# Kernel tuning notes

Hardware: AMD Instinct MI355X
Metric: run time of the kernel (lower is better)

Reference implementation:

```python
import jax, jax.numpy as jnp
import numpy as np

N, S, F, E, H, O, L, FE = 8, 1024, 64, 512, 8, 64, 6, 4
HD = E // H
FF = FE * E


def setup_inputs() -> dict:
    key = jax.random.key(0)
    ks = iter(jax.random.split(key, 40))
    def rn(shape, s=0.02):
        return jax.random.normal(next(ks), shape, jnp.float32) * s
    return {
        'x': jax.random.normal(next(ks), (N, F, S), jnp.float32),
        'W_first': rn((F, E)), 'b_first': jnp.zeros((E,), jnp.float32),
        'pos_emb': rn((S, E)),
        'Wq': rn((L, HD, HD)), 'bq': jnp.zeros((L, HD), jnp.float32),
        'Wk': rn((L, HD, HD)), 'bk': jnp.zeros((L, HD), jnp.float32),
        'Wv': rn((L, HD, HD)), 'bv': jnp.zeros((L, HD), jnp.float32),
        'Wo': rn((L, E, E)), 'bo': jnp.zeros((L, E), jnp.float32),
        'g1': jnp.ones((L, E), jnp.float32), 'be1': jnp.zeros((L, E), jnp.float32),
        'Wf1': rn((L, E, FF)), 'bf1': jnp.zeros((L, FF), jnp.float32),
        'Wf2': rn((L, FF, E)), 'bf2': jnp.zeros((L, E), jnp.float32),
        'g2': jnp.ones((L, E), jnp.float32), 'be2': jnp.zeros((L, E), jnp.float32),
        'Wfin': rn((E, O)), 'bfin': jnp.zeros((O,), jnp.float32),
    }


def layernorm(x, g, b, eps=1e-5):
    m = jnp.mean(x, axis=-1, keepdims=True)
    v = jnp.mean(jnp.square(x - m), axis=-1, keepdims=True)
    return (x - m) * jax.lax.rsqrt(v + eps) * g + b


def reference(x, W_first, b_first, pos_emb, Wq, bq, Wk, bk, Wv, bv, Wo, bo,
              g1, be1, Wf1, bf1, Wf2, bf2, g2, be2, Wfin, bfin):
    # x: (N, F, S) -> (N, S, F)
    h = jax.nn.relu(jnp.einsum('nfs,fe->nse', x, W_first) + b_first) + pos_emb[None]
    scale = E ** 0.5  # note: module scales by sqrt(embed_size), not sqrt(head_dim)
    for i in range(L):
        t = h.reshape(N, S, H, HD)
        q = jnp.einsum('nshd,de->nshe', t, Wq[i]) + bq[i]
        k = jnp.einsum('nshd,de->nshe', t, Wk[i]) + bk[i]
        v = jnp.einsum('nshd,de->nshe', t, Wv[i]) + bv[i]
        energy = jnp.einsum('nqhd,nkhd->nhqk', q, k)  # (N,H,S,S)
        att = jax.nn.softmax(energy / scale, axis=-1)
        o = jnp.einsum('nhqk,nkhd->nqhd', att, v).reshape(N, S, E)
        o = jnp.einsum('nse,ef->nsf', o, Wo[i]) + bo[i]
        hx = layernorm(o + h, g1[i], be1[i])
        ff = jax.nn.relu(jnp.einsum('nse,ef->nsf', hx, Wf1[i]) + bf1[i])
        ff = jnp.einsum('nsf,fe->nse', ff, Wf2[i]) + bf2[i]
        h = layernorm(ff + hx, g2[i], be2[i])
    # Conv1d kernel_size=1 == pointwise linear over channels; output (N, O, S)
    return jnp.einsum('nse,eo->nos', h, Wfin) + bfin[None, :, None]
```

## Files before the change

kernel.cpp:

```cpp
#include <hip/hip_runtime.h>
#include <hip/hip_bf16.h>
#include <math.h>

#define N_ 8
#define S_ 1024
#define F_ 64
#define E_ 512
#define H_ 8
#define O_ 64
#define L_ 6
#define HD_ 64
#define FF_ 2048
#define SCALE_ 0.044194173824159216f
#define LOG2E_ 1.4426950408889634f
#define QSCALE_ (SCALE_ * LOG2E_)

typedef unsigned short u16;
typedef __attribute__((ext_vector_type(4))) unsigned short u16x4;
typedef __attribute__((ext_vector_type(8))) unsigned short u16x8;
typedef __attribute__((ext_vector_type(8))) short short8;
typedef __attribute__((ext_vector_type(4))) float floatx4;

__device__ __forceinline__ u16 f2b(float f) {
    union { float f; unsigned u; } v; v.f = f;
    unsigned u = v.u;
    unsigned r = (u + 0x7FFFu + ((u >> 16) & 1u)) >> 16;
    return (u16)r;
}
__device__ __forceinline__ u16 f2b_fast(float f) {
    union { float f; unsigned u; } v; v.f = f;
    return (u16)((v.u + 0x8000u) >> 16);
}
__device__ __forceinline__ float b2f(u16 h) {
    union { unsigned u; float f; } v; v.u = ((unsigned)h) << 16;
    return v.f;
}

__device__ __forceinline__ void gload16(const u16* g, u16* l) {
    __builtin_amdgcn_global_load_lds(
        (const __attribute__((address_space(1))) void*)g,
        (__attribute__((address_space(3))) void*)l, 16, 0, 0);
}

__global__ __launch_bounds__(256) void first_mfma(
    const float* __restrict__ x, const u16* __restrict__ wt,
    const float* __restrict__ bf, const float* __restrict__ pe,
    u16* __restrict__ resb)
{
    __shared__ u16 a_s[128][72];
    int t = threadIdx.x;
    int w = t >> 6, lane = t & 63, quad = lane >> 4, c16 = lane & 15;
    int rowhalf = w >> 1, colhalf = w & 1;
    int col0 = blockIdx.x * 128;
    int row0 = blockIdx.y * 128;
    int n = row0 >> 10, s0 = row0 & 1023;

    const float* xb = x + (size_t)n * F_ * S_ + s0;
    #pragma unroll
    for (int i = 0; i < 8; i++) {
        int pos = (t + i * 256) * 4;
        int f = pos >> 7, sl = pos & 127;
        float4 v = *(const float4*)&xb[(size_t)f * S_ + sl];
        a_s[sl + 0][f] = f2b_fast(v.x);
        a_s[sl + 1][f] = f2b_fast(v.y);
        a_s[sl + 2][f] = f2b_fast(v.z);
        a_s[sl + 3][f] = f2b_fast(v.w);
    }
    __syncthreads();

    floatx4 acc[4][4];
    #pragma unroll
    for (int mt = 0; mt < 4; mt++)
        #pragma unroll
        for (int nt = 0; nt < 4; nt++) acc[mt][nt] = (floatx4){0.f, 0.f, 0.f, 0.f};

    #pragma unroll
    for (int ks = 0; ks < 2; ks++) {
        short8 af[4], bfr[4];
        #pragma unroll
        for (int mt = 0; mt < 4; mt++)
            af[mt] = *(const short8*)&a_s[rowhalf * 64 + mt * 16 + c16][ks * 32 + quad * 8];
        #pragma unroll
        for (int nt = 0; nt < 4; nt++)
            bfr[nt] = *(const short8*)&wt[(size_t)(col0 + colhalf * 64 + nt * 16 + c16) * F_
                                          + ks * 32 + quad * 8];
        #pragma unroll
        for (int mt = 0; mt < 4; mt++)
            #pragma unroll
            for (int nt = 0; nt < 4; nt++)
                acc[mt][nt] = __builtin_amdgcn_mfma_f32_16x16x32_bf16(
                    af[mt], bfr[nt], acc[mt][nt], 0, 0, 0);
    }

    #pragma unroll
    for (int nt = 0; nt < 4; nt++) {
        int col = col0 + colhalf * 64 + nt * 16 + c16;
        float bv = bf[col];
        #pragma unroll
        for (int mt = 0; mt < 4; mt++) {
            #pragma unroll
            for (int r = 0; r < 4; r++) {
                size_t row = (size_t)row0 + rowhalf * 64 + mt * 16 + quad * 4 + r;
                int s = (int)(row & 1023);
                float v = fmaxf(acc[mt][nt][r] + bv, 0.f) + pe[(size_t)s * E_ + col];
                resb[row * E_ + col] = f2b_fast(v);
            }
        }
    }
}

__global__ __launch_bounds__(256) void wprep(
    const float* __restrict__ W_first, const float* __restrict__ Wo,
    const float* __restrict__ Wf1, const float* __restrict__ Wf2,
    const float* __restrict__ Wfin,
    const float* __restrict__ Wq, const float* __restrict__ Wk,
    const float* __restrict__ Wv,
    u16* __restrict__ w1t, u16* __restrict__ wot, u16* __restrict__ wf1t,
    u16* __restrict__ wf2t, u16* __restrict__ wft,
    u16* __restrict__ wqt, u16* __restrict__ wkt, u16* __restrict__ wvt)
{
    int b = blockIdx.x;
    int t = threadIdx.x;
    __shared__ float tile[32][33];
    const float* W; u16* Wt; int K, Nc, bx, by;
    if (b < 32) {
        W = W_first; Wt = w1t; K = F_; Nc = E_; bx = b & 15; by = b >> 4;
    } else if (b < 32 + 1536) {
        int i = b - 32; int z = i >> 8; int r = i & 255;
        W = Wo + (size_t)z * E_ * E_; Wt = wot + (size_t)z * E_ * E_;
        K = E_; Nc = E_; bx = r & 15; by = r >> 4;
    } else if (b < 32 + 1536 + 6144) {
        int i = b - (32 + 1536); int z = i >> 10; int r = i & 1023;
        W = Wf1 + (size_t)z * E_ * FF_; Wt = wf1t + (size_t)z * E_ * FF_;
        K = E_; Nc = FF_; bx = r & 63; by = r >> 6;
    } else if (b < 32 + 1536 + 12288) {
        int i = b - (32 + 1536 + 6144); int z = i >> 10; int r = i & 1023;
        W = Wf2 + (size_t)z * FF_ * E_; Wt = wf2t + (size_t)z * FF_ * E_;
        K = FF_; Nc = E_; bx = r & 15; by = r >> 4;
    } else if (b < 32 + 1536 + 12288 + 32) {
        int r = b - (32 + 1536 + 12288);
        W = Wfin; Wt = wft; K = E_; Nc = O_; bx = r & 1; by = r >> 1;
    } else {
        int l = b - (32 + 1536 + 12288 + 32);
        size_t off = (size_t)l * HD_ * HD_;
        #pragma unroll
        for (int i = 0; i < 16; i++) {
            int idx = t + i * 256;
            int e = idx >> 6, d = idx & 63;
            wqt[off + idx] = f2b(Wq[off + d * HD_ + e]);
            wkt[off + idx] = f2b(Wk[off + d * HD_ + e]);
            wvt[off + idx] = f2b(Wv[off + d * HD_ + e]);
        }
        return;
    }
    #pragma unroll
    for (int i = 0; i < 4; i++) {
        int q = t + i * 256; int r = q >> 5, c = q & 31;
        tile[r][c] = W[(size_t)(by * 32 + r) * Nc + bx * 32 + c];
    }
    __syncthreads();
    #pragma unroll
    for (int i = 0; i < 4; i++) {
        int q = t + i * 256; int r = q >> 5, c = q & 31;
        Wt[(size_t)(bx * 32 + r) * K + by * 32 + c] = f2b(tile[c][r]);
    }
}

__global__ __launch_bounds__(256) void qkv_mfma(
    const u16* __restrict__ hb,
    const u16* __restrict__ wqt, const u16* __restrict__ wkt,
    const u16* __restrict__ wvt,
    const float* __restrict__ bq, const float* __restrict__ bk,
    const float* __restrict__ bvp,
    u16* __restrict__ qo, u16* __restrict__ ko, u16* __restrict__ vt)
{
    __shared__ u16 a_s[128 * 64];
    int t = threadIdx.x;
    int w = t >> 6, lane = t & 63, quad = lane >> 4, c16 = lane & 15;
    size_t row0 = (size_t)blockIdx.x * 128;

    #pragma unroll
    for (int i = 0; i < 4; i++) {
        int q = t + i * 256; int r = q >> 3, c = q & 7;
        *(u16x8*)&a_s[r * 64 + ((c ^ (r & 7)) * 8)] =
            *(const u16x8*)&hb[(row0 + r) * HD_ + c * 8];
    }
    __syncthreads();

    short8 af[2][2];
    #pragma unroll
    for (int mt = 0; mt < 2; mt++)
        #pragma unroll
        for (int ks = 0; ks < 2; ks++) {
            int r = w * 32 + mt * 16 + c16;
            af[mt][ks] = *(const short8*)&a_s[r * 64 + (((ks * 4 + quad) ^ (r & 7)) * 8)];
        }

    const u16* wts[2] = {wqt, wkt};
    const float* bs[2] = {bq, bk};
    u16* outs[2] = {qo, ko};
    #pragma unroll
    for (int m = 0; m < 2; m++) {
        short8 bfr[4][2];
        #pragma unroll
        for (int nt = 0; nt < 4; nt++)
            #pragma unroll
            for (int ks = 0; ks < 2; ks++)
                bfr[nt][ks] = *(const short8*)&wts[m][(nt * 16 + c16) * HD_ + ks * 32 + quad * 8];
        floatx4 acc[2][4];
        #pragma unroll
        for (int mt = 0; mt < 2; mt++)
            #pragma unroll
            for (int nt = 0; nt < 4; nt++) acc[mt][nt] = (floatx4){0.f, 0.f, 0.f, 0.f};
        #pragma unroll
        for (int ks = 0; ks < 2; ks++)
            #pragma unroll
            for (int mt = 0; mt < 2; mt++)
                #pragma unroll
                for (int nt = 0; nt < 4; nt++)
                    acc[mt][nt] = __builtin_amdgcn_mfma_f32_16x16x32_bf16(
                        af[mt][ks], bfr[nt][ks], acc[mt][nt], 0, 0, 0);
        float osc = (m == 0) ? QSCALE_ : 1.0f;
        #pragma unroll
        for (int nt = 0; nt < 4; nt++) {
            float bv_ = bs[m][nt * 16 + c16];
            #pragma unroll
            for (int mt = 0; mt < 2; mt++)
                #pragma unroll
                for (int r = 0; r < 4; r++)
                    outs[m][(row0 + w * 32 + mt * 16 + quad * 4 + r) * HD_ + nt * 16 + c16] =
                        f2b_fast((acc[mt][nt][r] + bv_) * osc);
        }
    }

    {
        short8 bfr[4][2];
        #pragma unroll
        for (int nt = 0; nt < 4; nt++)
            #pragma unroll
            for (int ks = 0; ks < 2; ks++)
                bfr[nt][ks] = *(const short8*)&wvt[(nt * 16 + c16) * HD_ + ks * 32 + quad * 8];
        floatx4 acc[2][4];
        #pragma unroll
        for (int mt = 0; mt < 2; mt++)
            #pragma unroll
            for (int nt = 0; nt < 4; nt++) acc[mt][nt] = (floatx4){0.f, 0.f, 0.f, 0.f};
        #pragma unroll
        for (int ks = 0; ks < 2; ks++)
            #pragma unroll
            for (int mt = 0; mt < 2; mt++)
                #pragma unroll
                for (int nt = 0; nt < 4; nt++)
                    acc[mt][nt] = __builtin_amdgcn_mfma_f32_16x16x32_bf16(
                        af[mt][ks], bfr[nt][ks], acc[mt][nt], 0, 0, 0);

        __syncthreads();
        u16* vt_s = a_s;
        #pragma unroll
        for (int nt = 0; nt < 4; nt++) {
            float bv_ = bvp[nt * 16 + c16];
            #pragma unroll
            for (int mt = 0; mt < 2; mt++)
                #pragma unroll
                for (int r = 0; r < 4; r++) {
                    int fr = w * 32 + mt * 16 + quad * 4 + r;
                    int h = fr & 7, sl = fr >> 3;
                    vt_s[((h * 64 + nt * 16 + c16) * 16) + sl] =
                        f2b_fast(acc[mt][nt][r] + bv_);
                }
        }
        __syncthreads();
        int sflat0 = (int)(row0 >> 3);
        int n = sflat0 >> 10, sbase = sflat0 & 1023;
        #pragma unroll
        for (int i = 0; i < 4; i++) {
            int u = t + i * 256;
            int h = u >> 7, rest = u & 127, d = rest >> 1, half = rest & 1;
            *(u16x8*)&vt[((size_t)((n * 8 + h) * 64 + d)) * (size_t)S_ + sbase + half * 8] =
                *(u16x8*)&vt_s[(h * 64 + d) * 16 + half * 8];
        }
    }
}

__global__ __launch_bounds__(256, 4) void attn_mfma(
    const u16* __restrict__ Q, const u16* __restrict__ K,
    const u16* __restrict__ Vt, u16* __restrict__ O)
{
    int bid0 = blockIdx.x;
    int bid = (bid0 & 7) * 128 + (bid0 >> 3);
    int qt = bid & 15, hh = (bid >> 4) & 7, n = bid >> 7;
    int t = threadIdx.x;
    int w = t >> 6, lane = t & 63, quad = lane >> 4, c16 = lane & 15;

    __shared__ u16 qp_s[64 * 64];
    __shared__ u16 k_s[2][64 * 64];
    __shared__ u16 vt_s[2][64 * 64];
    u16* p_s = qp_s + w * 16 * 64;

    const size_t qkbase = (size_t)n * S_ * E_ + hh * 64;
    const size_t vtbase = ((size_t)(n * H_ + hh) * 64) * (size_t)S_;

    int ar = t >> 3, act = t & 7;
    int acq = act * 8;
    int scw[2];
    #pragma unroll
    for (int i = 0; i < 2; i++) scw[i] = ((act ^ ((ar + i * 32) & 7)) * 8);

    #pragma unroll
    for (int i = 0; i < 2; i++) {
        int q = t + i * 256; int r = q >> 3, c = q & 7;
        *(u16x8*)&qp_s[r * 64 + ((c ^ (r & 7)) * 8)] =
            *(const u16x8*)&Q[qkbase + (size_t)(qt * 64 + r) * E_ + c * 8];
    }
    u16x8 pk[2], pv[2];
    #pragma unroll
    for (int i = 0; i < 2; i++) {
        pk[i] = *(const u16x8*)&K[qkbase + (size_t)(ar + i * 32) * E_ + acq];
        pv[i] = *(const u16x8*)&Vt[vtbase + (size_t)(ar + i * 32) * S_ + acq];
    }
    __syncthreads();

    short8 qf[2];
    #pragma unroll
    for (int ks = 0; ks < 2; ks++) {
        int r = w * 16 + c16;
        qf[ks] = *(const short8*)&qp_s[r * 64 + (((ks * 4 + quad) ^ (r & 7)) * 8)];
    }

    #pragma unroll
    for (int i = 0; i < 2; i++) {
        int r = ar + i * 32;
        *(u16x8*)&k_s[0][r * 64 + scw[i]] = pk[i];
        *(u16x8*)&vt_s[0][r * 64 + scw[i]] = pv[i];
    }
    __syncthreads();

    const short8 ones = {(short)0x3F80, (short)0x3F80, (short)0x3F80, (short)0x3F80,
                         (short)0x3F80, (short)0x3F80, (short)0x3F80, (short)0x3F80};

    floatx4 oaccT[4];
    floatx4 lacc = (floatx4){0.f, 0.f, 0.f, 0.f};
    #pragma unroll
    for (int mt = 0; mt < 4; mt++) oaccT[mt] = (floatx4){0.f, 0.f, 0.f, 0.f};

    for (int k0 = 0; k0 < S_; k0 += 64) {
        int cur = (k0 >> 6) & 1;
        const u16* ks_ = k_s[cur];
        const u16* vs_ = vt_s[cur];
        bool more = (k0 + 64 < S_);
        if (more) {
            #pragma unroll
            for (int i = 0; i < 2; i++) {
                pk[i] = *(const u16x8*)&K[qkbase + (size_t)(k0 + 64 + ar + i * 32) * E_ + acq];
                pv[i] = *(const u16x8*)&Vt[vtbase + (size_t)(ar + i * 32) * S_ + k0 + 64 + acq];
            }
        }

        floatx4 st[4];
        #pragma unroll
        for (int mt = 0; mt < 4; mt++) st[mt] = (floatx4){0.f, 0.f, 0.f, 0.f};
        __builtin_amdgcn_s_setprio(1);
        #pragma unroll
        for (int ks = 0; ks < 2; ks++) {
            short8 kf[4];
            #pragma unroll
            for (int mt = 0; mt < 4; mt++) {
                int r = mt * 16 + c16;
                kf[mt] = *(const short8*)&ks_[r * 64 + (((ks * 4 + quad) ^ (r & 7)) * 8)];
            }
            #pragma unroll
            for (int mt = 0; mt < 4; mt++)
                st[mt] = __builtin_amdgcn_mfma_f32_16x16x32_bf16(
                    kf[mt], qf[ks], st[mt], 0, 0, 0);
        }
        __builtin_amdgcn_s_setprio(0);

        #pragma unroll
        for (int mt = 0; mt < 4; mt++) {
            u16x4 h;
            #pragma unroll
            for (int r = 0; r < 4; r++) h[r] = f2b_fast(exp2f(st[mt][r]));
            *(u16x4*)&p_s[c16 * 64 + (((2 * mt + (quad >> 1)) ^ (c16 & 7)) * 8)
                          + (quad & 1) * 4] = h;
        }

        __builtin_amdgcn_s_setprio(1);
        #pragma unroll
        for (int ks = 0; ks < 2; ks++) {
            short8 pf = *(const short8*)&p_s[c16 * 64 + (((ks * 4 + quad) ^ (c16 & 7)) * 8)];
            short8 vf[4];
            #pragma unroll
            for (int mt = 0; mt < 4; mt++) {
                int r = mt * 16 + c16;
                vf[mt] = *(const short8*)&vs_[r * 64 + (((ks * 4 + quad) ^ (r & 7)) * 8)];
            }
            lacc = __builtin_amdgcn_mfma_f32_16x16x32_bf16(ones, pf, lacc, 0, 0, 0);
            #pragma unroll
            for (int mt = 0; mt < 4; mt++)
                oaccT[mt] = __builtin_amdgcn_mfma_f32_16x16x32_bf16(
                    vf[mt], pf, oaccT[mt], 0, 0, 0);
        }
        __builtin_amdgcn_s_setprio(0);

        if (more) {
            u16* kd = k_s[cur ^ 1];
            u16* vd = vt_s[cur ^ 1];
            #pragma unroll
            for (int i = 0; i < 2; i++) {
                int r = ar + i * 32;
                *(u16x8*)&kd[r * 64 + scw[i]] = pk[i];
                *(u16x8*)&vd[r * 64 + scw[i]] = pv[i];
            }
        }
        __syncthreads();
    }

    {
        float rl = 1.f / lacc[0];
        int s = qt * 64 + w * 16 + c16;
        size_t base = (size_t)(n * S_ + s) * E_ + hh * 64;
        #pragma unroll
        for (int mt = 0; mt < 4; mt++) {
            u16x4 h;
            #pragma unroll
            for (int r = 0; r < 4; r++) h[r] = f2b_fast(oaccT[mt][r] * rl);
            *(u16x4*)&O[base + mt * 16 + quad * 4] = h;
        }
    }
}

template <int MT, int NT, bool RELU, bool HASRES, bool OUTF32, bool OUTBF16>
__global__ __launch_bounds__(256, 2) void gemm_mfma(
    const u16* __restrict__ A, const u16* __restrict__ Bt,
    const float* __restrict__ bias, const u16* __restrict__ resid,
    float* __restrict__ outf, u16* __restrict__ outb, int M, int Nc, int K)
{
    constexpr int MFR = MT / 32;
    constexpr int NFR = NT / 32;
    constexpr int AI  = MT / 32;
    constexpr int BI  = NT / 32;
    __shared__ u16 a_s[MT * 64];
    __shared__ u16 b_s[NT * 64];

    int t = threadIdx.x;
    int w = t >> 6, lane = t & 63, quad = lane >> 4, c16 = lane & 15;
    int rw = w >> 1, cw = w & 1;

    int gx = gridDim.x;
    int nwg = gx * (int)gridDim.y;
    int lin = (int)blockIdx.y * gx + (int)blockIdx.x;
    int cpx = nwg >> 3;
    int id2 = (lin & 7) * cpx + (lin >> 3);
    int bx = id2 % gx, by = id2 / gx;

    size_t row0 = (size_t)by * MT;
    size_t col0 = (size_t)bx * NT;

    size_t aoff[AI]; int adst[AI];
    #pragma unroll
    for (int i = 0; i < AI; i++) {
        int p = t + i * 256;
        int r = p >> 3;
        int kc = (p & 7) ^ (r & 7);
        aoff[i] = (row0 + r) * (size_t)K + kc * 8;
        adst[i] = w * 512 + i * 2048;
    }
    size_t boff[BI]; int bdst[BI];
    #pragma unroll
    for (int i = 0; i < BI; i++) {
        int p = t + i * 256;
        int r = p >> 3;
        int kc = (p & 7) ^ (r & 7);
        boff[i] = (col0 + r) * (size_t)K + kc * 8;
        bdst[i] = w * 512 + i * 2048;
    }

    floatx4 acc[MFR][NFR];
    #pragma unroll
    for (int mt = 0; mt < MFR; mt++)
        #pragma unroll
        for (int nt = 0; nt < NFR; nt++) acc[mt][nt] = (floatx4){0.f, 0.f, 0.f, 0.f};

    for (int k0 = 0; k0 < K; k0 += 64) {
        #pragma unroll
        for (int i = 0; i < AI; i++) gload16(A + aoff[i] + k0, a_s + adst[i]);
        #pragma unroll
        for (int i = 0; i < BI; i++) gload16(Bt + boff[i] + k0, b_s + bdst[i]);
        __syncthreads();

        #pragma unroll
        for (int ks = 0; ks < 2; ks++) {
            short8 af[MFR], bfr[NFR];
            #pragma unroll
            for (int mt = 0; mt < MFR; mt++) {
                int r = rw * (MT / 2) + mt * 16 + c16;
                af[mt] = *(const short8*)&a_s[r * 64 + (((ks * 4 + quad) ^ (r & 7)) * 8)];
            }
            #pragma unroll
            for (int nt = 0; nt < NFR; nt++) {
                int r = cw * (NT / 2) + nt * 16 + c16;
                bfr[nt] = *(const short8*)&b_s[r * 64 + (((ks * 4 + quad) ^ (r & 7)) * 8)];
            }
            #pragma unroll
            for (int mt = 0; mt < MFR; mt++)
                #pragma unroll
                for (int nt = 0; nt < NFR; nt++)
                    acc[mt][nt] = __builtin_amdgcn_mfma_f32_16x16x32_bf16(
                        af[mt], bfr[nt], acc[mt][nt], 0, 0, 0);
        }
        __syncthreads();
    }

    #pragma unroll
    for (int nt = 0; nt < NFR; nt++) {
        int col = (int)col0 + cw * (NT / 2) + nt * 16 + c16;
        float bv = bias[col];
        #pragma unroll
        for (int mt = 0; mt < MFR; mt++) {
            size_t rowb = row0 + rw * (MT / 2) + mt * 16 + quad * 4;
            #pragma unroll
            for (int r = 0; r < 4; r++) {
                size_t row = rowb + r;
                float v = acc[mt][nt][r] + bv;
                if constexpr (HASRES) v += b2f(resid[row * Nc + col]);
                if constexpr (RELU) v = fmaxf(v, 0.f);
                if constexpr (OUTF32) outf[row * Nc + col] = v;
                if constexpr (OUTBF16) outb[row * Nc + col] = f2b_fast(v);
            }
        }
    }
}

__global__ __launch_bounds__(256) void layernorm_k(
    const float* __restrict__ in, const float* __restrict__ g,
    const float* __restrict__ bb, u16* __restrict__ outb)
{
    int row = blockIdx.x;
    int t = threadIdx.x;
    const float* x = in + (size_t)row * E_;
    float x0 = x[t], x1 = x[t + 256];
    float s = x0 + x1;
    #pragma unroll
    for (int off = 32; off; off >>= 1) s += __shfl_down(s, off, 64);
    __shared__ float red[4];
    int wid = t >> 6, lane = t & 63;
    if (lane == 0) red[wid] = s;
    __syncthreads();
    float m = (red[0] + red[1] + red[2] + red[3]) * (1.f / E_);
    float d0 = x0 - m, d1 = x1 - m;
    float sq = d0 * d0 + d1 * d1;
    #pragma unroll
    for (int off = 32; off; off >>= 1) sq += __shfl_down(sq, off, 64);
    __syncthreads();
    if (lane == 0) red[wid] = sq;
    __syncthreads();
    float var = (red[0] + red[1] + red[2] + red[3]) * (1.f / E_);
    float rstd = rsqrtf(var + 1e-5f);
    outb[(size_t)row * E_ + t] = f2b_fast(d0 * rstd * g[t] + bb[t]);
    outb[(size_t)row * E_ + t + 256] = f2b_fast(d1 * rstd * g[t + 256] + bb[t + 256]);
}

__global__ __launch_bounds__(256) void final_mfma(
    const u16* __restrict__ hb, const u16* __restrict__ wft,
    const float* __restrict__ bfin, float* __restrict__ outp)
{
    __shared__ u16 a_s[64][72];
    int t = threadIdx.x;
    int w = t >> 6, lane = t & 63, quad = lane >> 4, c16 = lane & 15;
    size_t row0 = (size_t)blockIdx.x * 64;

    floatx4 acc[4];
    #pragma unroll
    for (int nt = 0; nt < 4; nt++) acc[nt] = (floatx4){0.f, 0.f, 0.f, 0.f};

    int ar = t >> 3, acq = (t & 7) * 8;
    u16x8 pa[2];
    #pragma unroll
    for (int i = 0; i < 2; i++)
        pa[i] = *(const u16x8*)&hb[(row0 + ar + i * 32) * E_ + acq];

    for (int k0 = 0; k0 < E_; k0 += 64) {
        #pragma unroll
        for (int i = 0; i < 2; i++)
            *(u16x8*)&a_s[ar + i * 32][acq] = pa[i];
        __syncthreads();
        if (k0 + 64 < E_) {
            #pragma unroll
            for (int i = 0; i < 2; i++)
                pa[i] = *(const u16x8*)&hb[(row0 + ar + i * 32) * E_ + k0 + 64 + acq];
        }
        #pragma unroll
        for (int ks = 0; ks < 2; ks++) {
            short8 af = *(const short8*)&a_s[w * 16 + c16][ks * 32 + quad * 8];
            #pragma unroll
            for (int nt = 0; nt < 4; nt++) {
                short8 bf = *(const short8*)&wft[(nt * 16 + c16) * E_ + k0 + ks * 32 + quad * 8];
                acc[nt] = __builtin_amdgcn_mfma_f32_16x16x32_bf16(af, bf, acc[nt], 0, 0, 0);
            }
        }
        __syncthreads();
    }

    #pragma unroll
    for (int nt = 0; nt < 4; nt++) {
        int o = nt * 16 + c16;
        float bv = bfin[o];
        #pragma unroll
        for (int r = 0; r < 4; r++) {
            size_t row = row0 + w * 16 + quad * 4 + r;
            int n = (int)(row >> 10), s = (int)(row & 1023);
            outp[((size_t)(n * O_ + o)) * S_ + s] = acc[nt][r] + bv;
        }
    }
}

extern "C" void kernel_launch(void* const* d_in, const int* in_sizes, int n_in,
                              void* d_out, int out_size, void* d_ws, size_t ws_size,
                              hipStream_t stream)
{
    const float* x       = (const float*)d_in[0];
    const float* W_first = (const float*)d_in[1];
    const float* b_first = (const float*)d_in[2];
    const float* pos_emb = (const float*)d_in[3];
    const float* Wq      = (const float*)d_in[4];
    const float* bq      = (const float*)d_in[5];
    const float* Wk      = (const float*)d_in[6];
    const float* bk      = (const float*)d_in[7];
    const float* Wv      = (const float*)d_in[8];
    const float* bv      = (const float*)d_in[9];
    const float* Wo      = (const float*)d_in[10];
    const float* bo      = (const float*)d_in[11];
    const float* g1      = (const float*)d_in[12];
    const float* be1     = (const float*)d_in[13];
    const float* Wf1     = (const float*)d_in[14];
    const float* bf1     = (const float*)d_in[15];
    const float* Wf2     = (const float*)d_in[16];
    const float* bf2     = (const float*)d_in[17];
    const float* g2      = (const float*)d_in[18];
    const float* be2     = (const float*)d_in[19];
    const float* Wfin    = (const float*)d_in[20];
    const float* bfin    = (const float*)d_in[21];
    float* out = (float*)d_out;

    const size_t M4 = (size_t)N_ * S_ * E_;
    float* t1   = (float*)d_ws;
    u16*   resb = (u16*)(t1 + M4);
    u16*   qb   = resb + M4;
    u16*   kb   = qb + M4;
    u16*   vt   = kb + M4;
    u16*   ob   = vt + M4;
    u16*   ffb  = qb;
    u16*   wot  = ob + M4;
    u16*   wf1t = wot + (size_t)L_ * E_ * E_;
    u16*   wf2t = wf1t + (size_t)L_ * E_ * FF_;
    u16*   wqt  = wf2t + (size_t)L_ * FF_ * E_;
    u16*   wkt  = wqt + (size_t)L_ * HD_ * HD_;
    u16*   wvt  = wkt + (size_t)L_ * HD_ * HD_;
    u16*   wft  = wvt + (size_t)L_ * HD_ * HD_;
    u16*   w1t  = wft + (size_t)O_ * E_;

    const int rows = N_ * S_;

    wprep<<<32 + 1536 + 12288 + 32 + 6, 256, 0, stream>>>(
        W_first, Wo, Wf1, Wf2, Wfin, Wq, Wk, Wv,
        w1t, wot, wf1t, wf2t, wft, wqt, wkt, wvt);

    first_mfma<<<dim3(E_ / 128, rows / 128), 256, 0, stream>>>(
        x, w1t, b_first, pos_emb, resb);

    for (int i = 0; i < L_; i++) {
        qkv_mfma<<<512, 256, 0, stream>>>(
            resb, wqt + (size_t)i * HD_ * HD_, wkt + (size_t)i * HD_ * HD_,
            wvt + (size_t)i * HD_ * HD_, bq + i * HD_, bk + i * HD_, bv + i * HD_,
            qb, kb, vt);
        attn_mfma<<<1024, 256, 0, stream>>>(qb, kb, vt, ob);
        gemm_mfma<128, 64, false, true, true, false><<<dim3(E_ / 64, rows / 128), 256, 0, stream>>>(
            ob, wot + (size_t)i * E_ * E_, bo + i * E_, resb, t1, nullptr, rows, E_, E_);
        layernorm_k<<<rows, 256, 0, stream>>>(t1, g1 + i * E_, be1 + i * E_, resb);
        gemm_mfma<128, 128, true, false, false, true><<<dim3(FF_ / 128, rows / 128), 256, 0, stream>>>(
            resb, wf1t + (size_t)i * E_ * FF_, bf1 + i * FF_, nullptr, nullptr, ffb,
            rows, FF_, E_);
        gemm_mfma<128, 64, false, true, true, false><<<dim3(E_ / 64, rows / 128), 256, 0, stream>>>(
            ffb, wf2t + (size_t)i * FF_ * E_, bf2 + i * E_, resb, t1, nullptr,
            rows, E_, FF_);
        layernorm_k<<<rows, 256, 0, stream>>>(t1, g2 + i * E_, be2 + i * E_, resb);
    }

    final_mfma<<<rows / 64, 256, 0, stream>>>(resb, wft, bfin, out);
}
```

Before: 1.005 ms.

## Double-buffer GEMM loads, widen attention blocks, vectorize layernorm, simplify QKV loads

The GEMM kernel now double-buffers its A/B shared tiles so the next K-slice loads are issued before the current slice's MFMAs, removing one barrier per iteration. Attention blocks grow to 512 threads covering 128 query rows, so each K/V tile staged in shared memory serves twice as many queries and each thread issues half as many tile loads. The QKV kernel reads its A fragments straight from global memory and no longer stages them in LDS, dropping a barrier. Layernorm uses float2 loads and packed bf16 stores. The costs are doubled GEMM shared memory, which may lower occupancy, and launch_bounds(512,4), which may constrain registers in the attention kernel.

```diff
diff --git a/kernel.cpp b/kernel.cpp
--- a/kernel.cpp
+++ b/kernel.cpp
@@ -174,27 +174,18 @@
     const float* __restrict__ bvp,
     u16* __restrict__ qo, u16* __restrict__ ko, u16* __restrict__ vt)
 {
-    __shared__ u16 a_s[128 * 64];
+    __shared__ u16 vt_s[128 * 64];
     int t = threadIdx.x;
     int w = t >> 6, lane = t & 63, quad = lane >> 4, c16 = lane & 15;
     size_t row0 = (size_t)blockIdx.x * 128;
 
-    #pragma unroll
-    for (int i = 0; i < 4; i++) {
-        int q = t + i * 256; int r = q >> 3, c = q & 7;
-        *(u16x8*)&a_s[r * 64 + ((c ^ (r & 7)) * 8)] =
-            *(const u16x8*)&hb[(row0 + r) * HD_ + c * 8];
-    }
-    __syncthreads();
-
     short8 af[2][2];
     #pragma unroll
     for (int mt = 0; mt < 2; mt++)
         #pragma unroll
-        for (int ks = 0; ks < 2; ks++) {
-            int r = w * 32 + mt * 16 + c16;
-            af[mt][ks] = *(const short8*)&a_s[r * 64 + (((ks * 4 + quad) ^ (r & 7)) * 8)];
-        }
+        for (int ks = 0; ks < 2; ks++)
+            af[mt][ks] = *(const short8*)&hb[(row0 + w * 32 + mt * 16 + c16) * HD_
+                                             + ks * 32 + quad * 8];
 
     const u16* wts[2] = {wqt, wkt};
     const float* bs[2] = {bq, bk};
@@ -254,8 +245,6 @@
                     acc[mt][nt] = __builtin_amdgcn_mfma_f32_16x16x32_bf16(
                         af[mt][ks], bfr[nt][ks], acc[mt][nt], 0, 0, 0);
 
-        __syncthreads();
-        u16* vt_s = a_s;
         #pragma unroll
         for (int nt = 0; nt < 4; nt++) {
             float bv_ = bvp[nt * 16 + c16];
@@ -282,17 +271,17 @@
     }
 }
 
-__global__ __launch_bounds__(256, 4) void attn_mfma(
+__global__ __launch_bounds__(512, 4) void attn_mfma(
     const u16* __restrict__ Q, const u16* __restrict__ K,
     const u16* __restrict__ Vt, u16* __restrict__ O)
 {
     int bid0 = blockIdx.x;
-    int bid = (bid0 & 7) * 128 + (bid0 >> 3);
-    int qt = bid & 15, hh = (bid >> 4) & 7, n = bid >> 7;
+    int bid = (bid0 & 7) * 64 + (bid0 >> 3);
+    int qt = bid & 7, hh = (bid >> 3) & 7, n = bid >> 6;
     int t = threadIdx.x;
     int w = t >> 6, lane = t & 63, quad = lane >> 4, c16 = lane & 15;
 
-    __shared__ u16 qp_s[64 * 64];
+    __shared__ u16 qp_s[128 * 64];
     __shared__ u16 k_s[2][64 * 64];
     __shared__ u16 vt_s[2][64 * 64];
     u16* p_s = qp_s + w * 16 * 64;
@@ -302,22 +291,16 @@
 
     int ar = t >> 3, act = t & 7;
     int acq = act * 8;
-    int scw[2];
-    #pragma unroll
-    for (int i = 0; i < 2; i++) scw[i] = ((act ^ ((ar + i * 32) & 7)) * 8);
+    int scw = (act ^ (ar & 7)) * 8;
 
     #pragma unroll
     for (int i = 0; i < 2; i++) {
-        int q = t + i * 256; int r = q >> 3, c = q & 7;
+        int q = t + i * 512; int r = q >> 3, c = q & 7;
         *(u16x8*)&qp_s[r * 64 + ((c ^ (r & 7)) * 8)] =
-            *(const u16x8*)&Q[qkbase + (size_t)(qt * 64 + r) * E_ + c * 8];
-    }
-    u16x8 pk[2], pv[2];
-    #pragma unroll
-    for (int i = 0; i < 2; i++) {
-        pk[i] = *(const u16x8*)&K[qkbase + (size_t)(ar + i * 32) * E_ + acq];
-        pv[i] = *(const u16x8*)&Vt[vtbase + (size_t)(ar + i * 32) * S_ + acq];
-    }
+            *(const u16x8*)&Q[qkbase + (size_t)(qt * 128 + r) * E_ + c * 8];
+    }
+    u16x8 pk = *(const u16x8*)&K[qkbase + (size_t)ar * E_ + acq];
+    u16x8 pv = *(const u16x8*)&Vt[vtbase + (size_t)ar * S_ + acq];
     __syncthreads();
 
     short8 qf[2];
@@ -327,12 +310,8 @@
         qf[ks] = *(const short8*)&qp_s[r * 64 + (((ks * 4 + quad) ^ (r & 7)) * 8)];
     }
 
-    #pragma unroll
-    for (int i = 0; i < 2; i++) {
-        int r = ar + i * 32;
-        *(u16x8*)&k_s[0][r * 64 + scw[i]] = pk[i];
-        *(u16x8*)&vt_s[0][r * 64 + scw[i]] = pv[i];
-    }
+    *(u16x8*)&k_s[0][ar * 64 + scw] = pk;
+    *(u16x8*)&vt_s[0][ar * 64 + scw] = pv;
     __syncthreads();
 
     const short8 ones = {(short)0x3F80, (short)0x3F80, (short)0x3F80, (short)0x3F80,
@@ -349,11 +328,8 @@
         const u16* vs_ = vt_s[cur];
         bool more = (k0 + 64 < S_);
         if (more) {
-            #pragma unroll
-            for (int i = 0; i < 2; i++) {
-                pk[i] = *(const u16x8*)&K[qkbase + (size_t)(k0 + 64 + ar + i * 32) * E_ + acq];
-                pv[i] = *(const u16x8*)&Vt[vtbase + (size_t)(ar + i * 32) * S_ + k0 + 64 + acq];
-            }
+            pk = *(const u16x8*)&K[qkbase + (size_t)(k0 + 64 + ar) * E_ + acq];
+            pv = *(const u16x8*)&Vt[vtbase + (size_t)ar * S_ + k0 + 64 + acq];
         }
 
         floatx4 st[4];
@@ -403,21 +379,15 @@
         __builtin_amdgcn_s_setprio(0);
 
         if (more) {
-            u16* kd = k_s[cur ^ 1];
-            u16* vd = vt_s[cur ^ 1];
-            #pragma unroll
-            for (int i = 0; i < 2; i++) {
-                int r = ar + i * 32;
-                *(u16x8*)&kd[r * 64 + scw[i]] = pk[i];
-                *(u16x8*)&vd[r * 64 + scw[i]] = pv[i];
-            }
+            *(u16x8*)&k_s[cur ^ 1][ar * 64 + scw] = pk;
+            *(u16x8*)&vt_s[cur ^ 1][ar * 64 + scw] = pv;
         }
         __syncthreads();
     }
 
     {
         float rl = 1.f / lacc[0];
-        int s = qt * 64 + w * 16 + c16;
+        int s = qt * 128 + w * 16 + c16;
         size_t base = (size_t)(n * S_ + s) * E_ + hh * 64;
         #pragma unroll
         for (int mt = 0; mt < 4; mt++) {
@@ -439,8 +409,8 @@
     constexpr int NFR = NT / 32;
     constexpr int AI  = MT / 32;
     constexpr int BI  = NT / 32;
-    __shared__ u16 a_s[MT * 64];
-    __shared__ u16 b_s[NT * 64];
+    __shared__ u16 a_s[2][MT * 64];
+    __shared__ u16 b_s[2][NT * 64];
 
     int t = threadIdx.x;
     int w = t >> 6, lane = t & 63, quad = lane >> 4, c16 = lane & 15;
@@ -481,12 +451,20 @@
         #pragma unroll
         for (int nt = 0; nt < NFR; nt++) acc[mt][nt] = (floatx4){0.f, 0.f, 0.f, 0.f};
 
+    #pragma unroll
+    for (int i = 0; i < AI; i++) gload16(A + aoff[i], &a_s[0][adst[i]]);
+    #pragma unroll
+    for (int i = 0; i < BI; i++) gload16(Bt + boff[i], &b_s[0][bdst[i]]);
+
     for (int k0 = 0; k0 < K; k0 += 64) {
-        #pragma unroll
-        for (int i = 0; i < AI; i++) gload16(A + aoff[i] + k0, a_s + adst[i]);
-        #pragma unroll
-        for (int i = 0; i < BI; i++) gload16(Bt + boff[i] + k0, b_s + bdst[i]);
+        int cur = (k0 >> 6) & 1;
         __syncthreads();
+        if (k0 + 64 < K) {
+            #pragma unroll
+            for (int i = 0; i < AI; i++) gload16(A + aoff[i] + k0 + 64, &a_s[cur ^ 1][adst[i]]);
+            #pragma unroll
+            for (int i = 0; i < BI; i++) gload16(Bt + boff[i] + k0 + 64, &b_s[cur ^ 1][bdst[i]]);
+        }
 
         #pragma unroll
         for (int ks = 0; ks < 2; ks++) {
@@ -494,12 +472,12 @@
             #pragma unroll
             for (int mt = 0; mt < MFR; mt++) {
                 int r = rw * (MT / 2) + mt * 16 + c16;
-                af[mt] = *(const short8*)&a_s[r * 64 + (((ks * 4 + quad) ^ (r & 7)) * 8)];
+                af[mt] = *(const short8*)&a_s[cur][r * 64 + (((ks * 4 + quad) ^ (r & 7)) * 8)];
             }
             #pragma unroll
             for (int nt = 0; nt < NFR; nt++) {
                 int r = cw * (NT / 2) + nt * 16 + c16;
-                bfr[nt] = *(const short8*)&b_s[r * 64 + (((ks * 4 + quad) ^ (r & 7)) * 8)];
+                bfr[nt] = *(const short8*)&b_s[cur][r * 64 + (((ks * 4 + quad) ^ (r & 7)) * 8)];
             }
             #pragma unroll
             for (int mt = 0; mt < MFR; mt++)
@@ -508,7 +486,6 @@
                     acc[mt][nt] = __builtin_amdgcn_mfma_f32_16x16x32_bf16(
                         af[mt], bfr[nt], acc[mt][nt], 0, 0, 0);
         }
-        __syncthreads();
     }
 
     #pragma unroll
@@ -538,8 +515,8 @@
     int row = blockIdx.x;
     int t = threadIdx.x;
     const float* x = in + (size_t)row * E_;
-    float x0 = x[t], x1 = x[t + 256];
-    float s = x0 + x1;
+    float2 xv = *(const float2*)&x[t * 2];
+    float s = xv.x + xv.y;
     #pragma unroll
     for (int off = 32; off; off >>= 1) s += __shfl_down(s, off, 64);
     __shared__ float red[4];
@@ -547,7 +524,7 @@
     if (lane == 0) red[wid] = s;
     __syncthreads();
     float m = (red[0] + red[1] + red[2] + red[3]) * (1.f / E_);
-    float d0 = x0 - m, d1 = x1 - m;
+    float d0 = xv.x - m, d1 = xv.y - m;
     float sq = d0 * d0 + d1 * d1;
     #pragma unroll
     for (int off = 32; off; off >>= 1) sq += __shfl_down(sq, off, 64);
@@ -556,8 +533,11 @@
     __syncthreads();
     float var = (red[0] + red[1] + red[2] + red[3]) * (1.f / E_);
     float rstd = rsqrtf(var + 1e-5f);
-    outb[(size_t)row * E_ + t] = f2b_fast(d0 * rstd * g[t] + bb[t]);
-    outb[(size_t)row * E_ + t + 256] = f2b_fast(d1 * rstd * g[t + 256] + bb[t + 256]);
+    float2 gv = *(const float2*)&g[t * 2];
+    float2 bv = *(const float2*)&bb[t * 2];
+    unsigned o = (unsigned)f2b_fast(d0 * rstd * gv.x + bv.x)
+               | ((unsigned)f2b_fast(d1 * rstd * gv.y + bv.y) << 16);
+    *(unsigned*)&outb[(size_t)row * E_ + t * 2] = o;
 }
 
 __global__ __launch_bounds__(256) void final_mfma(
@@ -673,7 +653,7 @@
             resb, wqt + (size_t)i * HD_ * HD_, wkt + (size_t)i * HD_ * HD_,
             wvt + (size_t)i * HD_ * HD_, bq + i * HD_, bk + i * HD_, bv + i * HD_,
             qb, kb, vt);
-        attn_mfma<<<1024, 256, 0, stream>>>(qb, kb, vt, ob);
+        attn_mfma<<<512, 512, 0, stream>>>(qb, kb, vt, ob);
         gemm_mfma<128, 64, false, true, true, false><<<dim3(E_ / 64, rows / 128), 256, 0, stream>>>(
             ob, wot + (size_t)i * E_ * E_, bo + i * E_, resb, t1, nullptr, rows, E_, E_);
         layernorm_k<<<rows, 256, 0, stream>>>(t1, g1 + i * E_, be1 + i * E_, resb);
```

Measured after the change: 958.4 us. -4.6%, faster.
